# Kernel optimization log

Measured on AMD Instinct MI355X. Metric: run time of the kernel, lower is better.

## Reference

```python
import math
import jax, jax.numpy as jnp
import numpy as np

B, T, C = 2, 2048, 1024
HEADS = 16
HD = C // HEADS  # 64


def setup_inputs() -> dict:
    key = jax.random.key(0)
    ks = jax.random.split(key, 5)
    s = 0.02
    return {
        "x": jax.random.normal(ks[0], (B, T, C), jnp.float32),
        "Wq": jax.random.normal(ks[1], (C, C), jnp.float32) * s,
        "bq": jnp.zeros((C,), jnp.float32),
        "Wk": jax.random.normal(ks[2], (C, HD), jnp.float32) * s,
        "bk": jnp.zeros((HD,), jnp.float32),
        "Wv": jax.random.normal(ks[3], (C, HD), jnp.float32) * s,
        "bv": jnp.zeros((HD,), jnp.float32),
        "Wo": jax.random.normal(ks[4], (C, C), jnp.float32) * s,
        "bo": jnp.zeros((C,), jnp.float32),
    }


def _rope_tables(seq_len, dim):
    pos = jnp.arange(seq_len, dtype=jnp.float32)
    freqs = 1.0 / (10000.0 ** (jnp.arange(0, dim, 2, dtype=jnp.float32) / dim))
    ang = pos[:, None] * freqs[None, :]          # (T, dim//2)
    # broadcast over (B, T, H, dim//2)
    return jnp.sin(ang)[None, :, None, :], jnp.cos(ang)[None, :, None, :]


def _apply_rope(t, sin, cos, dim):
    t1, t2 = t[..., : dim // 2], t[..., dim // 2 :]
    # matches torch source: emb[..., :d/2]=sin, emb[..., d/2:]=cos
    return jnp.concatenate([t1 * cos + t2 * sin, t1 * sin - t2 * cos], axis=-1)


def reference(x, Wq, bq, Wk, bk, Wv, bv, Wo, bo):
    Bx, Tx, Cx = x.shape
    q = (x @ Wq + bq).reshape(Bx, Tx, HEADS, HD)   # (B,T,H,hd)
    k = (x @ Wk + bk)[:, :, None, :]               # (B,T,1,hd) single KV head (MQA)
    v = (x @ Wv + bv)[:, :, None, :]
    sin, cos = _rope_tables(Tx, HD)
    q = _apply_rope(q, sin, cos, HD)
    k = _apply_rope(k, sin, cos, HD)
    att = jnp.einsum('bthd,bThd->bhtT', q, k) / math.sqrt(HD)
    causal = jnp.triu(jnp.ones((Tx, Tx), bool), 1)
    att = jnp.where(causal, -jnp.inf, att)
    att = jax.nn.softmax(att, axis=-1)
    out = jnp.einsum('bhtT,bThd->bthd', att, v).reshape(Bx, Tx, Cx)
    return out @ Wo + bo
```

## Files before the change

kernel.cpp:

```cpp
#include <hip/hip_runtime.h>
#include <math.h>

#define BSZ   2
#define TSEQ  2048
#define CDIM  1024
#define NHEAD 16
#define HDIM  64
#define BT    (BSZ*TSEQ)
#define NQKV  1152

typedef __attribute__((ext_vector_type(8))) short short8;
typedef __attribute__((ext_vector_type(4))) float f32x4;
typedef unsigned short u16;
typedef unsigned int   u32;

__device__ __forceinline__ u16 f2b(float f) {
    union { float f; u32 u; } c; c.f = f;
    u32 u = c.u;
    u += 0x7fffu + ((u >> 16) & 1u);
    return (u16)(u >> 16);
}
__device__ __forceinline__ u32 pack2(float lo, float hi) {
    return (u32)f2b(lo) | ((u32)f2b(hi) << 16);
}

__device__ __forceinline__ void async_copy16(const void* g, void* l) {
    __builtin_amdgcn_global_load_lds(
        (__attribute__((address_space(1))) const void*)g,
        (__attribute__((address_space(3))) void*)l,
        16, 0, 0);
}

__global__ __launch_bounds__(256) void cast_bf16_kernel(
    const float* __restrict__ src, u16* __restrict__ dst, int n4)
{
    int i = blockIdx.x * 256 + threadIdx.x;
    if (i >= n4) return;
    float4 f = ((const float4*)src)[i];
    u16* d = dst + (size_t)i * 4;
    d[0] = f2b(f.x); d[1] = f2b(f.y); d[2] = f2b(f.z); d[3] = f2b(f.w);
}

__device__ __forceinline__ void transpose_tile(
    const float* __restrict__ W, u16* __restrict__ Wt,
    int K, int Nw, int nofs, int bx, int by, float (*T)[65])
{
    const int tid = threadIdx.x;
    const int k0 = by * 64, n0 = bx * 64;
    #pragma unroll
    for (int i = 0; i < 16; ++i) {
        int idx = i * 256 + tid, r = idx >> 6, c = idx & 63;
        T[r][c] = W[(size_t)(k0 + r) * Nw + n0 + c];
    }
    __syncthreads();
    #pragma unroll
    for (int i = 0; i < 16; ++i) {
        int idx = i * 256 + tid, rn = idx >> 6, ck = idx & 63;
        Wt[(size_t)(nofs + n0 + rn) * K + k0 + ck] = f2b(T[ck][rn]);
    }
}

__global__ __launch_bounds__(256) void prep_kernel(
    const float* __restrict__ Wq, const float* __restrict__ Wk,
    const float* __restrict__ Wv, const float* __restrict__ Wo,
    const float* __restrict__ bq, const float* __restrict__ bk,
    const float* __restrict__ bv,
    u16* __restrict__ Wqkvt, u16* __restrict__ Wot, float* __restrict__ bqkv)
{
    __shared__ float T[64][65];
    const int bid = blockIdx.x;
    if (bid < 256) {
        transpose_tile(Wq, Wqkvt, 1024, 1024, 0, bid & 15, bid >> 4, T);
    } else if (bid < 272) {
        transpose_tile(Wk, Wqkvt, 1024, 64, 1024, 0, bid - 256, T);
    } else if (bid < 288) {
        transpose_tile(Wv, Wqkvt, 1024, 64, 1088, 0, bid - 272, T);
    } else if (bid < 544) {
        int b2 = bid - 288;
        transpose_tile(Wo, Wot, 1024, 1024, 0, b2 & 15, b2 >> 4, T);
    } else {
        for (int i = threadIdx.x; i < NQKV; i += 256)
            bqkv[i] = (i < 1024) ? bq[i] : (i < 1088 ? bk[i - 1024] : bv[i - 1088]);
    }
}

__global__ __launch_bounds__(256) void gemm_qkv_kernel(
    const u16* __restrict__ A, const u16* __restrict__ Bt,
    const float* __restrict__ bias,
    u16* __restrict__ qb, u16* __restrict__ kb, u16* __restrict__ vT)
{
    __shared__ __align__(16) u16 AsC[64 * 32];
    __shared__ __align__(16) u16 BsC[128 * 32];
    const int tid  = threadIdx.x;
    const int wave = tid >> 6, lane = tid & 63;
    const int ln16 = lane & 15, quad = lane >> 4;
    const int wm = wave >> 1, wn = wave & 1;
    const int m0 = blockIdx.y * 64, n0 = blockIdx.x * 128;
    const int K = CDIM;

    const int c_row = ((tid >> 6) << 4) + (tid & 15);
    const int c_k   = ((tid >> 4) & 3) * 8;
    const u16* ag  = &A [(size_t)(m0 + c_row)       * K + c_k];
    const u16* bg0 = &Bt[(size_t)(n0 + c_row)       * K + c_k];
    const u16* bg1 = &Bt[(size_t)(n0 + 64 + c_row)  * K + c_k];
    u16* a_l  = &AsC[(size_t)wave * 64 * 8];
    u16* b_l0 = &BsC[(size_t)wave * 64 * 8];
    u16* b_l1 = &BsC[(size_t)(wave + 4) * 64 * 8];

    f32x4 acc[2][4];
    #pragma unroll
    for (int i = 0; i < 2; ++i)
        #pragma unroll
        for (int j = 0; j < 4; ++j) acc[i][j] = (f32x4){0.f, 0.f, 0.f, 0.f};

    for (int k0 = 0; k0 < K; k0 += 32) {
        async_copy16(ag,  a_l);
        async_copy16(bg0, b_l0);
        async_copy16(bg1, b_l1);
        ag += 32; bg0 += 32; bg1 += 32;
        __syncthreads();

        short8 af[2], bf[4];
        #pragma unroll
        for (int mt = 0; mt < 2; ++mt)
            af[mt] = *(const short8*)&AsC[(((wm * 2 + mt) * 64) + quad * 16 + ln16) * 8];
        #pragma unroll
        for (int nt = 0; nt < 4; ++nt)
            bf[nt] = *(const short8*)&BsC[(((wn * 4 + nt) * 64) + quad * 16 + ln16) * 8];
        #pragma unroll
        for (int mt = 0; mt < 2; ++mt)
            #pragma unroll
            for (int nt = 0; nt < 4; ++nt)
                acc[mt][nt] = __builtin_amdgcn_mfma_f32_16x16x32_bf16(
                    af[mt], bf[nt], acc[mt][nt], 0, 0, 0);
        __syncthreads();
    }

    #pragma unroll
    for (int mt = 0; mt < 2; ++mt)
        #pragma unroll
        for (int nt = 0; nt < 4; ++nt) {
            float bb = bias[n0 + wn * 64 + nt * 16 + ln16];
            #pragma unroll
            for (int r = 0; r < 4; ++r) acc[mt][nt][r] += bb;
        }

    const int col0 = n0 + wn * 64;
    if (col0 < 1024) {
        const int hh = col0 >> 6;
        #pragma unroll
        for (int nt = 0; nt < 2; ++nt) {
            int j = nt * 16 + ln16;
            float fr = exp2f(-0.41524101186092029f * (float)j);
            #pragma unroll
            for (int mt = 0; mt < 2; ++mt)
                #pragma unroll
                for (int r = 0; r < 4; ++r) {
                    int m = m0 + wm * 32 + mt * 16 + quad * 4 + r;
                    float sn, cs;
                    __sincosf((float)(m & (TSEQ - 1)) * fr, &sn, &cs);
                    float t1 = acc[mt][nt][r], t2 = acc[mt][nt + 2][r];
                    u16* o = qb + (size_t)m * CDIM + hh * 64 + j;
                    o[0]  = f2b(fmaf(t1, cs,  t2 * sn) * 0.125f);
                    o[32] = f2b(fmaf(t1, sn, -t2 * cs) * 0.125f);
                }
        }
    } else if (wn == 0) {
        #pragma unroll
        for (int nt = 0; nt < 2; ++nt) {
            int j = nt * 16 + ln16;
            float fr = exp2f(-0.41524101186092029f * (float)j);
            #pragma unroll
            for (int mt = 0; mt < 2; ++mt)
                #pragma unroll
                for (int r = 0; r < 4; ++r) {
                    int m = m0 + wm * 32 + mt * 16 + quad * 4 + r;
                    float sn, cs;
                    __sincosf((float)(m & (TSEQ - 1)) * fr, &sn, &cs);
                    float t1 = acc[mt][nt][r], t2 = acc[mt][nt + 2][r];
                    u16* o = kb + (size_t)m * HDIM + j;
                    o[0]  = f2b(fmaf(t1, cs,  t2 * sn));
                    o[32] = f2b(fmaf(t1, sn, -t2 * cs));
                }
        }
    } else {
        #pragma unroll
        for (int nt = 0; nt < 4; ++nt) {
            int d = nt * 16 + ln16;
            #pragma unroll
            for (int mt = 0; mt < 2; ++mt) {
                int mr = m0 + wm * 32 + mt * 16 + quad * 4;
                int b  = mr >> 11, tq = mr & (TSEQ - 1);
                uint2 val;
                val.x = pack2(acc[mt][nt][0], acc[mt][nt][1]);
                val.y = pack2(acc[mt][nt][2], acc[mt][nt][3]);
                *(uint2*)&vT[(size_t)(b * HDIM + d) * TSEQ + tq] = val;
            }
        }
    }
}

__global__ __launch_bounds__(256) void gemm_mfma_kernel(
    const u16* __restrict__ A, const u16* __restrict__ Bt,
    const float* __restrict__ bias, float* __restrict__ Y,
    int M, int N, int K)
{
    __shared__ __align__(16) u16 AsC[64 * 32];
    __shared__ __align__(16) u16 BsC[128 * 32];
    const int tid  = threadIdx.x;
    const int wave = tid >> 6, lane = tid & 63;
    const int ln16 = lane & 15, quad = lane >> 4;
    const int wm = wave >> 1, wn = wave & 1;
    const int m0 = blockIdx.y * 64, n0 = blockIdx.x * 128;

    const int c_row = ((tid >> 6) << 4) + (tid & 15);
    const int c_k   = ((tid >> 4) & 3) * 8;
    const u16* ag  = &A [(size_t)(m0 + c_row)       * K + c_k];
    const u16* bg0 = &Bt[(size_t)(n0 + c_row)       * K + c_k];
    const u16* bg1 = &Bt[(size_t)(n0 + 64 + c_row)  * K + c_k];
    u16* a_l  = &AsC[(size_t)wave * 64 * 8];
    u16* b_l0 = &BsC[(size_t)wave * 64 * 8];
    u16* b_l1 = &BsC[(size_t)(wave + 4) * 64 * 8];

    f32x4 acc[2][4];
    #pragma unroll
    for (int i = 0; i < 2; ++i)
        #pragma unroll
        for (int j = 0; j < 4; ++j) acc[i][j] = (f32x4){0.f, 0.f, 0.f, 0.f};

    for (int k0 = 0; k0 < K; k0 += 32) {
        async_copy16(ag,  a_l);
        async_copy16(bg0, b_l0);
        async_copy16(bg1, b_l1);
        ag += 32; bg0 += 32; bg1 += 32;
        __syncthreads();

        short8 af[2], bf[4];
        #pragma unroll
        for (int mt = 0; mt < 2; ++mt)
            af[mt] = *(const short8*)&AsC[(((wm * 2 + mt) * 64) + quad * 16 + ln16) * 8];
        #pragma unroll
        for (int nt = 0; nt < 4; ++nt)
            bf[nt] = *(const short8*)&BsC[(((wn * 4 + nt) * 64) + quad * 16 + ln16) * 8];
        #pragma unroll
        for (int mt = 0; mt < 2; ++mt)
            #pragma unroll
            for (int nt = 0; nt < 4; ++nt)
                acc[mt][nt] = __builtin_amdgcn_mfma_f32_16x16x32_bf16(
                    af[mt], bf[nt], acc[mt][nt], 0, 0, 0);
        __syncthreads();
    }

    #pragma unroll
    for (int mt = 0; mt < 2; ++mt)
        #pragma unroll
        for (int nt = 0; nt < 4; ++nt) {
            int n = n0 + wn * 64 + nt * 16 + ln16;
            float bb = bias[n];
            #pragma unroll
            for (int r = 0; r < 4; ++r) {
                int m = m0 + wm * 32 + mt * 16 + quad * 4 + r;
                Y[(size_t)m * N + n] = acc[mt][nt][r] + bb;
            }
        }
}

__global__ __launch_bounds__(256) void flash_mfma_kernel(
    const u16* __restrict__ qb, const u16* __restrict__ kb,
    const u16* __restrict__ vT, u16* __restrict__ o)
{
    const int id = blockIdx.x;
    const int p  = id & 15;
    const int h  = (id >> 4) & 15;
    const int b  = id >> 8;
    __shared__ __align__(16) u16 Qs[512 * 8];
    __shared__ __align__(16) u16 Ks[512 * 8];
    __shared__ __align__(16) u16 Vs[512 * 8];
    __shared__ __align__(16) u16 Ps[4 * 16 * 72];

    const int tid  = threadIdx.x;
    const int wave = tid >> 6, lane = tid & 63;
    const int ln16 = lane & 15, quad = lane >> 4;

    const int c0 = tid;
    int row_c[2], off_c[2];
    #pragma unroll
    for (int hf = 0; hf < 2; ++hf) {
        int c = c0 + hf * 256;
        row_c[hf] = ((c >> 7) << 4) | (c & 15);
        off_c[hf] = ((c >> 6) & 1) * 32 + ((c >> 4) & 3) * 8;
    }

    u16* Pw = &Ps[wave * 16 * 72];

    for (int s = 0; s < 2; ++s) {
        const int qt = s ? (31 - p) : p;

        #pragma unroll
        for (int hf = 0; hf < 2; ++hf)
            async_copy16(
                qb + (size_t)(b * TSEQ + qt * 64 + row_c[hf]) * CDIM + h * HDIM + off_c[hf],
                Qs + (c0 + hf * 256) * 8);

        float lsum[4];
        f32x4 oacc[4];
        #pragma unroll
        for (int r = 0; r < 4; ++r) lsum[r] = 0.f;
        #pragma unroll
        for (int t = 0; t < 4; ++t) oacc[t] = (f32x4){0.f, 0.f, 0.f, 0.f};

        for (int kt = 0; kt <= qt; ++kt) {
            const size_t kt0 = (size_t)(b * TSEQ + kt * 64);
            #pragma unroll
            for (int hf = 0; hf < 2; ++hf) {
                int cc = c0 + hf * 256;
                async_copy16(kb + (kt0 + row_c[hf]) * HDIM + off_c[hf], Ks + cc * 8);
                async_copy16(vT + (size_t)(b * HDIM + row_c[hf]) * TSEQ + kt * 64 + off_c[hf],
                             Vs + cc * 8);
            }
            __syncthreads();

            f32x4 sv[4];
            #pragma unroll
            for (int t = 0; t < 4; ++t) sv[t] = (f32x4){0.f, 0.f, 0.f, 0.f};
            #pragma unroll
            for (int kk2 = 0; kk2 < 2; ++kk2) {
                short8 af = *(const short8*)&Qs[(wave * 128 + kk2 * 64 + quad * 16 + ln16) * 8];
                #pragma unroll
                for (int t = 0; t < 4; ++t) {
                    short8 bf = *(const short8*)&Ks[(t * 128 + kk2 * 64 + quad * 16 + ln16) * 8];
                    sv[t] = __builtin_amdgcn_mfma_f32_16x16x32_bf16(af, bf, sv[t], 0, 0, 0);
                }
            }

            if (kt == qt) {
                #pragma unroll
                for (int t = 0; t < 4; ++t) {
                    int key = t * 16 + ln16;
                    #pragma unroll
                    for (int r = 0; r < 4; ++r) {
                        float e = (key > wave * 16 + quad * 4 + r)
                                    ? 0.f : __expf(sv[t][r]);
                        lsum[r] += e;
                        Pw[(quad * 4 + r) * 72 + t * 16 + ln16] = f2b(e);
                    }
                }
            } else {
                #pragma unroll
                for (int t = 0; t < 4; ++t)
                    #pragma unroll
                    for (int r = 0; r < 4; ++r) {
                        float e = __expf(sv[t][r]);
                        lsum[r] += e;
                        Pw[(quad * 4 + r) * 72 + t * 16 + ln16] = f2b(e);
                    }
            }

            #pragma unroll
            for (int kk2 = 0; kk2 < 2; ++kk2) {
                short8 pf = *(const short8*)&Pw[ln16 * 72 + kk2 * 32 + quad * 8];
                #pragma unroll
                for (int t = 0; t < 4; ++t) {
                    short8 vf = *(const short8*)&Vs[(t * 128 + kk2 * 64 + quad * 16 + ln16) * 8];
                    oacc[t] = __builtin_amdgcn_mfma_f32_16x16x32_bf16(pf, vf, oacc[t], 0, 0, 0);
                }
            }
            __syncthreads();
        }

        float inv[4];
        #pragma unroll
        for (int r = 0; r < 4; ++r) {
            float l = lsum[r];
            #pragma unroll
            for (int off = 1; off < 16; off <<= 1)
                l += __shfl_xor(l, off, 64);
            inv[r] = 1.0f / l;
        }
        #pragma unroll
        for (int t = 0; t < 4; ++t) {
            #pragma unroll
            for (int r = 0; r < 4; ++r) {
                int row = qt * 64 + wave * 16 + quad * 4 + r;
                int d   = t * 16 + ln16;
                o[(size_t)(b * TSEQ + row) * CDIM + h * HDIM + d] = f2b(oacc[t][r] * inv[r]);
            }
        }
    }
}

extern "C" void kernel_launch(void* const* d_in, const int* in_sizes, int n_in,
                              void* d_out, int out_size, void* d_ws, size_t ws_size,
                              hipStream_t stream)
{
    const float* x  = (const float*)d_in[0];
    const float* Wq = (const float*)d_in[1];
    const float* bq = (const float*)d_in[2];
    const float* Wk = (const float*)d_in[3];
    const float* bk = (const float*)d_in[4];
    const float* Wv = (const float*)d_in[5];
    const float* bv = (const float*)d_in[6];
    const float* Wo = (const float*)d_in[7];
    const float* bo = (const float*)d_in[8];
    float* out = (float*)d_out;

    const size_t MB = 1u << 20;
    char* w = (char*)d_ws;
    u16*   xb   = (u16*)(w);
    u16*   aob  = (u16*)(w);
    u16*   qb   = (u16*)(w + 8 * MB);
    u16*   kb   = (u16*)(w + 16 * MB);
    u16*   vT   = (u16*)(w + 16 * MB + 512 * 1024);
    u16*   Wqkvt= (u16*)(w + 17 * MB);
    u16*   Wot  = (u16*)(w + 20 * MB);
    float* bqkv = (float*)(w + 22 * MB);

    dim3 blk(256);

    cast_bf16_kernel<<<dim3(BT * CDIM / 4 / 256), blk, 0, stream>>>(x, xb, BT * CDIM / 4);
    prep_kernel<<<dim3(545), blk, 0, stream>>>(Wq, Wk, Wv, Wo, bq, bk, bv,
                                               Wqkvt, Wot, bqkv);
    gemm_qkv_kernel<<<dim3(NQKV / 128, BT / 64), blk, 0, stream>>>(
        xb, Wqkvt, bqkv, qb, kb, vT);
    flash_mfma_kernel<<<dim3(16 * NHEAD * BSZ), blk, 0, stream>>>(qb, kb, vT, aob);
    gemm_mfma_kernel<<<dim3(CDIM / 128, BT / 64), blk, 0, stream>>>(
        aob, Wot, bo, out, BT, CDIM, CDIM);
}
```

Before: 205.0 us.

## Shrink GEMM tiles to 64x64 with 2 waves and split flash work per query tile

Both GEMM kernels move from a 64x128 tile with 4 waves to a 64x64 tile with 2 waves, which doubles the block count so the 256 CUs are better filled. The flash attention kernel stops pairing a short and a long query tile in one block. It now launches one block per query tile, ordered longest-first to help load balance. In exchange, each GEMM block reuses less data, there are more launch blocks, and per-block causal work becomes uneven, which relies on the longest-first scheduling.

```diff
diff --git a/kernel.cpp b/kernel.cpp
--- a/kernel.cpp
+++ b/kernel.cpp
@@ -84,28 +84,31 @@
     }
 }
 
-__global__ __launch_bounds__(256) void gemm_qkv_kernel(
+__global__ __launch_bounds__(128) void gemm_qkv_kernel(
     const u16* __restrict__ A, const u16* __restrict__ Bt,
     const float* __restrict__ bias,
     u16* __restrict__ qb, u16* __restrict__ kb, u16* __restrict__ vT)
 {
     __shared__ __align__(16) u16 AsC[64 * 32];
-    __shared__ __align__(16) u16 BsC[128 * 32];
+    __shared__ __align__(16) u16 BsC[64 * 32];
     const int tid  = threadIdx.x;
     const int wave = tid >> 6, lane = tid & 63;
     const int ln16 = lane & 15, quad = lane >> 4;
-    const int wm = wave >> 1, wn = wave & 1;
-    const int m0 = blockIdx.y * 64, n0 = blockIdx.x * 128;
+    const int m0 = blockIdx.y * 64, n0 = blockIdx.x * 64;
     const int K = CDIM;
 
-    const int c_row = ((tid >> 6) << 4) + (tid & 15);
-    const int c_k   = ((tid >> 4) & 3) * 8;
-    const u16* ag  = &A [(size_t)(m0 + c_row)       * K + c_k];
-    const u16* bg0 = &Bt[(size_t)(n0 + c_row)       * K + c_k];
-    const u16* bg1 = &Bt[(size_t)(n0 + 64 + c_row)  * K + c_k];
-    u16* a_l  = &AsC[(size_t)wave * 64 * 8];
-    u16* b_l0 = &BsC[(size_t)wave * 64 * 8];
-    u16* b_l1 = &BsC[(size_t)(wave + 4) * 64 * 8];
+    const u16* ag[2]; u16* al[2];
+    const u16* bg[2]; u16* bl[2];
+    #pragma unroll
+    for (int n = 0; n < 2; ++n) {
+        int ca = tid + n * 128;
+        int row  = ((ca >> 6) << 4) | (ca & 15);
+        int koff = ((ca >> 4) & 3) * 8;
+        ag[n] = A  + (size_t)(m0 + row) * K + koff;
+        al[n] = AsC + ca * 8;
+        bg[n] = Bt + (size_t)(n0 + row) * K + koff;
+        bl[n] = BsC + ca * 8;
+    }
 
     f32x4 acc[2][4];
     #pragma unroll
@@ -114,19 +117,20 @@
         for (int j = 0; j < 4; ++j) acc[i][j] = (f32x4){0.f, 0.f, 0.f, 0.f};
 
     for (int k0 = 0; k0 < K; k0 += 32) {
-        async_copy16(ag,  a_l);
-        async_copy16(bg0, b_l0);
-        async_copy16(bg1, b_l1);
-        ag += 32; bg0 += 32; bg1 += 32;
+        #pragma unroll
+        for (int n = 0; n < 2; ++n) {
+            async_copy16(ag[n], al[n]); ag[n] += 32;
+            async_copy16(bg[n], bl[n]); bg[n] += 32;
+        }
         __syncthreads();
 
         short8 af[2], bf[4];
         #pragma unroll
         for (int mt = 0; mt < 2; ++mt)
-            af[mt] = *(const short8*)&AsC[(((wm * 2 + mt) * 64) + quad * 16 + ln16) * 8];
+            af[mt] = *(const short8*)&AsC[(((wave * 2 + mt) * 64) + lane) * 8];
         #pragma unroll
         for (int nt = 0; nt < 4; ++nt)
-            bf[nt] = *(const short8*)&BsC[(((wn * 4 + nt) * 64) + quad * 16 + ln16) * 8];
+            bf[nt] = *(const short8*)&BsC[((nt * 64) + lane) * 8];
         #pragma unroll
         for (int mt = 0; mt < 2; ++mt)
             #pragma unroll
@@ -137,17 +141,16 @@
     }
 
     #pragma unroll
-    for (int mt = 0; mt < 2; ++mt)
-        #pragma unroll
-        for (int nt = 0; nt < 4; ++nt) {
-            float bb = bias[n0 + wn * 64 + nt * 16 + ln16];
+    for (int nt = 0; nt < 4; ++nt) {
+        float bb = bias[n0 + nt * 16 + ln16];
+        #pragma unroll
+        for (int mt = 0; mt < 2; ++mt)
             #pragma unroll
             for (int r = 0; r < 4; ++r) acc[mt][nt][r] += bb;
-        }
-
-    const int col0 = n0 + wn * 64;
-    if (col0 < 1024) {
-        const int hh = col0 >> 6;
+    }
+
+    if (n0 < 1024) {
+        const int hh = n0 >> 6;
         #pragma unroll
         for (int nt = 0; nt < 2; ++nt) {
             int j = nt * 16 + ln16;
@@ -156,7 +159,7 @@
             for (int mt = 0; mt < 2; ++mt)
                 #pragma unroll
                 for (int r = 0; r < 4; ++r) {
-                    int m = m0 + wm * 32 + mt * 16 + quad * 4 + r;
+                    int m = m0 + wave * 32 + mt * 16 + quad * 4 + r;
                     float sn, cs;
                     __sincosf((float)(m & (TSEQ - 1)) * fr, &sn, &cs);
                     float t1 = acc[mt][nt][r], t2 = acc[mt][nt + 2][r];
@@ -165,7 +168,7 @@
                     o[32] = f2b(fmaf(t1, sn, -t2 * cs) * 0.125f);
                 }
         }
-    } else if (wn == 0) {
+    } else if (n0 == 1024) {
         #pragma unroll
         for (int nt = 0; nt < 2; ++nt) {
             int j = nt * 16 + ln16;
@@ -174,7 +177,7 @@
             for (int mt = 0; mt < 2; ++mt)
                 #pragma unroll
                 for (int r = 0; r < 4; ++r) {
-                    int m = m0 + wm * 32 + mt * 16 + quad * 4 + r;
+                    int m = m0 + wave * 32 + mt * 16 + quad * 4 + r;
                     float sn, cs;
                     __sincosf((float)(m & (TSEQ - 1)) * fr, &sn, &cs);
                     float t1 = acc[mt][nt][r], t2 = acc[mt][nt + 2][r];
@@ -189,7 +192,7 @@
             int d = nt * 16 + ln16;
             #pragma unroll
             for (int mt = 0; mt < 2; ++mt) {
-                int mr = m0 + wm * 32 + mt * 16 + quad * 4;
+                int mr = m0 + wave * 32 + mt * 16 + quad * 4;
                 int b  = mr >> 11, tq = mr & (TSEQ - 1);
                 uint2 val;
                 val.x = pack2(acc[mt][nt][0], acc[mt][nt][1]);
@@ -200,27 +203,30 @@
     }
 }
 
-__global__ __launch_bounds__(256) void gemm_mfma_kernel(
+__global__ __launch_bounds__(128) void gemm_mfma_kernel(
     const u16* __restrict__ A, const u16* __restrict__ Bt,
     const float* __restrict__ bias, float* __restrict__ Y,
     int M, int N, int K)
 {
     __shared__ __align__(16) u16 AsC[64 * 32];
-    __shared__ __align__(16) u16 BsC[128 * 32];
+    __shared__ __align__(16) u16 BsC[64 * 32];
     const int tid  = threadIdx.x;
     const int wave = tid >> 6, lane = tid & 63;
     const int ln16 = lane & 15, quad = lane >> 4;
-    const int wm = wave >> 1, wn = wave & 1;
-    const int m0 = blockIdx.y * 64, n0 = blockIdx.x * 128;
-
-    const int c_row = ((tid >> 6) << 4) + (tid & 15);
-    const int c_k   = ((tid >> 4) & 3) * 8;
-    const u16* ag  = &A [(size_t)(m0 + c_row)       * K + c_k];
-    const u16* bg0 = &Bt[(size_t)(n0 + c_row)       * K + c_k];
-    const u16* bg1 = &Bt[(size_t)(n0 + 64 + c_row)  * K + c_k];
-    u16* a_l  = &AsC[(size_t)wave * 64 * 8];
-    u16* b_l0 = &BsC[(size_t)wave * 64 * 8];
-    u16* b_l1 = &BsC[(size_t)(wave + 4) * 64 * 8];
+    const int m0 = blockIdx.y * 64, n0 = blockIdx.x * 64;
+
+    const u16* ag[2]; u16* al[2];
+    const u16* bg[2]; u16* bl[2];
+    #pragma unroll
+    for (int n = 0; n < 2; ++n) {
+        int ca = tid + n * 128;
+        int row  = ((ca >> 6) << 4) | (ca & 15);
+        int koff = ((ca >> 4) & 3) * 8;
+        ag[n] = A  + (size_t)(m0 + row) * K + koff;
+        al[n] = AsC + ca * 8;
+        bg[n] = Bt + (size_t)(n0 + row) * K + koff;
+        bl[n] = BsC + ca * 8;
+    }
 
     f32x4 acc[2][4];
     #pragma unroll
@@ -229,19 +235,20 @@
         for (int j = 0; j < 4; ++j) acc[i][j] = (f32x4){0.f, 0.f, 0.f, 0.f};
 
     for (int k0 = 0; k0 < K; k0 += 32) {
-        async_copy16(ag,  a_l);
-        async_copy16(bg0, b_l0);
-        async_copy16(bg1, b_l1);
-        ag += 32; bg0 += 32; bg1 += 32;
+        #pragma unroll
+        for (int n = 0; n < 2; ++n) {
+            async_copy16(ag[n], al[n]); ag[n] += 32;
+            async_copy16(bg[n], bl[n]); bg[n] += 32;
+        }
         __syncthreads();
 
         short8 af[2], bf[4];
         #pragma unroll
         for (int mt = 0; mt < 2; ++mt)
-            af[mt] = *(const short8*)&AsC[(((wm * 2 + mt) * 64) + quad * 16 + ln16) * 8];
+            af[mt] = *(const short8*)&AsC[(((wave * 2 + mt) * 64) + lane) * 8];
         #pragma unroll
         for (int nt = 0; nt < 4; ++nt)
-            bf[nt] = *(const short8*)&BsC[(((wn * 4 + nt) * 64) + quad * 16 + ln16) * 8];
+            bf[nt] = *(const short8*)&BsC[((nt * 64) + lane) * 8];
         #pragma unroll
         for (int mt = 0; mt < 2; ++mt)
             #pragma unroll
@@ -252,27 +259,28 @@
     }
 
     #pragma unroll
-    for (int mt = 0; mt < 2; ++mt)
-        #pragma unroll
-        for (int nt = 0; nt < 4; ++nt) {
-            int n = n0 + wn * 64 + nt * 16 + ln16;
-            float bb = bias[n];
+    for (int nt = 0; nt < 4; ++nt) {
+        int n = n0 + nt * 16 + ln16;
+        float bb = bias[n];
+        #pragma unroll
+        for (int mt = 0; mt < 2; ++mt)
             #pragma unroll
             for (int r = 0; r < 4; ++r) {
-                int m = m0 + wm * 32 + mt * 16 + quad * 4 + r;
+                int m = m0 + wave * 32 + mt * 16 + quad * 4 + r;
                 Y[(size_t)m * N + n] = acc[mt][nt][r] + bb;
             }
-        }
+    }
 }
 
 __global__ __launch_bounds__(256) void flash_mfma_kernel(
     const u16* __restrict__ qb, const u16* __restrict__ kb,
     const u16* __restrict__ vT, u16* __restrict__ o)
 {
-    const int id = blockIdx.x;
-    const int p  = id & 15;
-    const int h  = (id >> 4) & 15;
-    const int b  = id >> 8;
+    const int id  = blockIdx.x;
+    const int qt  = 31 - (id >> 5);
+    const int hb  = id & 31;
+    const int h   = hb >> 1;
+    const int b   = hb & 1;
     __shared__ __align__(16) u16 Qs[512 * 8];
     __shared__ __align__(16) u16 Ks[512 * 8];
     __shared__ __align__(16) u16 Vs[512 * 8];
@@ -293,98 +301,94 @@
 
     u16* Pw = &Ps[wave * 16 * 72];
 
-    for (int s = 0; s < 2; ++s) {
-        const int qt = s ? (31 - p) : p;
-
-        #pragma unroll
-        for (int hf = 0; hf < 2; ++hf)
-            async_copy16(
-                qb + (size_t)(b * TSEQ + qt * 64 + row_c[hf]) * CDIM + h * HDIM + off_c[hf],
-                Qs + (c0 + hf * 256) * 8);
-
-        float lsum[4];
-        f32x4 oacc[4];
-        #pragma unroll
-        for (int r = 0; r < 4; ++r) lsum[r] = 0.f;
-        #pragma unroll
-        for (int t = 0; t < 4; ++t) oacc[t] = (f32x4){0.f, 0.f, 0.f, 0.f};
-
-        for (int kt = 0; kt <= qt; ++kt) {
-            const size_t kt0 = (size_t)(b * TSEQ + kt * 64);
-            #pragma unroll
-            for (int hf = 0; hf < 2; ++hf) {
-                int cc = c0 + hf * 256;
-                async_copy16(kb + (kt0 + row_c[hf]) * HDIM + off_c[hf], Ks + cc * 8);
-                async_copy16(vT + (size_t)(b * HDIM + row_c[hf]) * TSEQ + kt * 64 + off_c[hf],
-                             Vs + cc * 8);
+    #pragma unroll
+    for (int hf = 0; hf < 2; ++hf)
+        async_copy16(
+            qb + (size_t)(b * TSEQ + qt * 64 + row_c[hf]) * CDIM + h * HDIM + off_c[hf],
+            Qs + (c0 + hf * 256) * 8);
+
+    float lsum[4];
+    f32x4 oacc[4];
+    #pragma unroll
+    for (int r = 0; r < 4; ++r) lsum[r] = 0.f;
+    #pragma unroll
+    for (int t = 0; t < 4; ++t) oacc[t] = (f32x4){0.f, 0.f, 0.f, 0.f};
+
+    for (int kt = 0; kt <= qt; ++kt) {
+        const size_t kt0 = (size_t)(b * TSEQ + kt * 64);
+        #pragma unroll
+        for (int hf = 0; hf < 2; ++hf) {
+            int cc = c0 + hf * 256;
+            async_copy16(kb + (kt0 + row_c[hf]) * HDIM + off_c[hf], Ks + cc * 8);
+            async_copy16(vT + (size_t)(b * HDIM + row_c[hf]) * TSEQ + kt * 64 + off_c[hf],
+                         Vs + cc * 8);
+        }
+        __syncthreads();
+
+        f32x4 sv[4];
+        #pragma unroll
+        for (int t = 0; t < 4; ++t) sv[t] = (f32x4){0.f, 0.f, 0.f, 0.f};
+        #pragma unroll
+        for (int kk2 = 0; kk2 < 2; ++kk2) {
+            short8 af = *(const short8*)&Qs[(wave * 128 + kk2 * 64 + quad * 16 + ln16) * 8];
+            #pragma unroll
+            for (int t = 0; t < 4; ++t) {
+                short8 bf = *(const short8*)&Ks[(t * 128 + kk2 * 64 + quad * 16 + ln16) * 8];
+                sv[t] = __builtin_amdgcn_mfma_f32_16x16x32_bf16(af, bf, sv[t], 0, 0, 0);
             }
-            __syncthreads();
-
-            f32x4 sv[4];
-            #pragma unroll
-            for (int t = 0; t < 4; ++t) sv[t] = (f32x4){0.f, 0.f, 0.f, 0.f};
-            #pragma unroll
-            for (int kk2 = 0; kk2 < 2; ++kk2) {
-                short8 af = *(const short8*)&Qs[(wave * 128 + kk2 * 64 + quad * 16 + ln16) * 8];
+        }
+
+        if (kt == qt) {
+            #pragma unroll
+            for (int t = 0; t < 4; ++t) {
+                int key = t * 16 + ln16;
                 #pragma unroll
-                for (int t = 0; t < 4; ++t) {
-                    short8 bf = *(const short8*)&Ks[(t * 128 + kk2 * 64 + quad * 16 + ln16) * 8];
-                    sv[t] = __builtin_amdgcn_mfma_f32_16x16x32_bf16(af, bf, sv[t], 0, 0, 0);
+                for (int r = 0; r < 4; ++r) {
+                    float e = (key > wave * 16 + quad * 4 + r)
+                                ? 0.f : __expf(sv[t][r]);
+                    lsum[r] += e;
+                    Pw[(quad * 4 + r) * 72 + t * 16 + ln16] = f2b(e);
                 }
             }
-
-            if (kt == qt) {
+        } else {
+            #pragma unroll
+            for (int t = 0; t < 4; ++t)
                 #pragma unroll
-                for (int t = 0; t < 4; ++t) {
-                    int key = t * 16 + ln16;
-                    #pragma unroll
-                    for (int r = 0; r < 4; ++r) {
-                        float e = (key > wave * 16 + quad * 4 + r)
-                                    ? 0.f : __expf(sv[t][r]);
-                        lsum[r] += e;
-                        Pw[(quad * 4 + r) * 72 + t * 16 + ln16] = f2b(e);
-                    }
+                for (int r = 0; r < 4; ++r) {
+                    float e = __expf(sv[t][r]);
+                    lsum[r] += e;
+                    Pw[(quad * 4 + r) * 72 + t * 16 + ln16] = f2b(e);
                 }
-            } else {
-                #pragma unroll
-                for (int t = 0; t < 4; ++t)
-                    #pragma unroll
-                    for (int r = 0; r < 4; ++r) {
-                        float e = __expf(sv[t][r]);
-                        lsum[r] += e;
-                        Pw[(quad * 4 + r) * 72 + t * 16 + ln16] = f2b(e);
-                    }
+        }
+
+        #pragma unroll
+        for (int kk2 = 0; kk2 < 2; ++kk2) {
+            short8 pf = *(const short8*)&Pw[ln16 * 72 + kk2 * 32 + quad * 8];
+            #pragma unroll
+            for (int t = 0; t < 4; ++t) {
+                short8 vf = *(const short8*)&Vs[(t * 128 + kk2 * 64 + quad * 16 + ln16) * 8];
+                oacc[t] = __builtin_amdgcn_mfma_f32_16x16x32_bf16(pf, vf, oacc[t], 0, 0, 0);
             }
-
-            #pragma unroll
-            for (int kk2 = 0; kk2 < 2; ++kk2) {
-                short8 pf = *(const short8*)&Pw[ln16 * 72 + kk2 * 32 + quad * 8];
-                #pragma unroll
-                for (int t = 0; t < 4; ++t) {
-                    short8 vf = *(const short8*)&Vs[(t * 128 + kk2 * 64 + quad * 16 + ln16) * 8];
-                    oacc[t] = __builtin_amdgcn_mfma_f32_16x16x32_bf16(pf, vf, oacc[t], 0, 0, 0);
-                }
-            }
-            __syncthreads();
-        }
-
-        float inv[4];
+        }
+        __syncthreads();
+    }
+
+    float inv[4];
+    #pragma unroll
+    for (int r = 0; r < 4; ++r) {
+        float l = lsum[r];
+        #pragma unroll
+        for (int off = 1; off < 16; off <<= 1)
+            l += __shfl_xor(l, off, 64);
+        inv[r] = 1.0f / l;
+    }
+    #pragma unroll
+    for (int t = 0; t < 4; ++t) {
         #pragma unroll
         for (int r = 0; r < 4; ++r) {
-            float l = lsum[r];
-            #pragma unroll
-            for (int off = 1; off < 16; off <<= 1)
-                l += __shfl_xor(l, off, 64);
-            inv[r] = 1.0f / l;
-        }
-        #pragma unroll
-        for (int t = 0; t < 4; ++t) {
-            #pragma unroll
-            for (int r = 0; r < 4; ++r) {
-                int row = qt * 64 + wave * 16 + quad * 4 + r;
-                int d   = t * 16 + ln16;
-                o[(size_t)(b * TSEQ + row) * CDIM + h * HDIM + d] = f2b(oacc[t][r] * inv[r]);
-            }
+            int row = qt * 64 + wave * 16 + quad * 4 + r;
+            int d   = t * 16 + ln16;
+            o[(size_t)(b * TSEQ + row) * CDIM + h * HDIM + d] = f2b(oacc[t][r] * inv[r]);
         }
     }
 }
@@ -415,14 +419,14 @@
     u16*   Wot  = (u16*)(w + 20 * MB);
     float* bqkv = (float*)(w + 22 * MB);
 
-    dim3 blk(256);
-
-    cast_bf16_kernel<<<dim3(BT * CDIM / 4 / 256), blk, 0, stream>>>(x, xb, BT * CDIM / 4);
-    prep_kernel<<<dim3(545), blk, 0, stream>>>(Wq, Wk, Wv, Wo, bq, bk, bv,
-                                               Wqkvt, Wot, bqkv);
-    gemm_qkv_kernel<<<dim3(NQKV / 128, BT / 64), blk, 0, stream>>>(
+    cast_bf16_kernel<<<dim3(BT * CDIM / 4 / 256), dim3(256), 0, stream>>>(
+        x, xb, BT * CDIM / 4);
+    prep_kernel<<<dim3(545), dim3(256), 0, stream>>>(Wq, Wk, Wv, Wo, bq, bk, bv,
+                                                     Wqkvt, Wot, bqkv);
+    gemm_qkv_kernel<<<dim3(NQKV / 64, BT / 64), dim3(128), 0, stream>>>(
         xb, Wqkvt, bqkv, qb, kb, vT);
-    flash_mfma_kernel<<<dim3(16 * NHEAD * BSZ), blk, 0, stream>>>(qb, kb, vT, aob);
-    gemm_mfma_kernel<<<dim3(CDIM / 128, BT / 64), blk, 0, stream>>>(
+    flash_mfma_kernel<<<dim3(32 * NHEAD * BSZ), dim3(256), 0, stream>>>(
+        qb, kb, vT, aob);
+    gemm_mfma_kernel<<<dim3(CDIM / 64, BT / 64), dim3(128), 0, stream>>>(
         aob, Wot, bo, out, BT, CDIM, CDIM);
 }
```

Result: slower. 212.4 us (+3.6%).

## Double-buffer K/V tiles in flash kernel and schedule one query tile per block

Applied to the files above, without the earlier changes.

Splits the flash attention work so each block handles a single query tile, launched longest-first, instead of a balanced pair of tiles per block. It adds a second K/V shared-memory buffer so the next tile's async copy overlaps the current tile's compute. It also folds log2(e) into the Q scale so exp2f replaces __expf. The trade-offs are more shared memory per block, twice as many blocks, and reliance on launch order to balance causal work.

```diff
diff --git a/kernel.cpp b/kernel.cpp
--- a/kernel.cpp
+++ b/kernel.cpp
@@ -161,8 +161,8 @@
                     __sincosf((float)(m & (TSEQ - 1)) * fr, &sn, &cs);
                     float t1 = acc[mt][nt][r], t2 = acc[mt][nt + 2][r];
                     u16* o = qb + (size_t)m * CDIM + hh * 64 + j;
-                    o[0]  = f2b(fmaf(t1, cs,  t2 * sn) * 0.125f);
-                    o[32] = f2b(fmaf(t1, sn, -t2 * cs) * 0.125f);
+                    o[0]  = f2b(fmaf(t1, cs,  t2 * sn) * 0.18033688011112043f);
+                    o[32] = f2b(fmaf(t1, sn, -t2 * cs) * 0.18033688011112043f);
                 }
         }
     } else if (wn == 0) {
@@ -265,17 +265,87 @@
         }
 }
 
+__device__ __forceinline__ void flash_stage_kv(
+    const u16* __restrict__ kb, const u16* __restrict__ vT,
+    int b, int kt, u16* __restrict__ Ksb, u16* __restrict__ Vsb,
+    const int* row_c, const int* off_c, int c0)
+{
+    const size_t kt0 = (size_t)(b * TSEQ + kt * 64);
+    #pragma unroll
+    for (int hf = 0; hf < 2; ++hf) {
+        int cc = c0 + hf * 256;
+        async_copy16(kb + (kt0 + row_c[hf]) * HDIM + off_c[hf], Ksb + cc * 8);
+        async_copy16(vT + (size_t)(b * HDIM + row_c[hf]) * TSEQ + kt * 64 + off_c[hf],
+                     Vsb + cc * 8);
+    }
+}
+
+__device__ __forceinline__ void flash_tile(
+    const u16* __restrict__ Ksb, const u16* __restrict__ Vsb,
+    const u16* __restrict__ Qs, u16* __restrict__ Pw,
+    int wave, int ln16, int quad, bool diag,
+    float* lsum, f32x4* oacc)
+{
+    f32x4 sv[4];
+    #pragma unroll
+    for (int t = 0; t < 4; ++t) sv[t] = (f32x4){0.f, 0.f, 0.f, 0.f};
+    #pragma unroll
+    for (int kk2 = 0; kk2 < 2; ++kk2) {
+        short8 af = *(const short8*)&Qs[(wave * 128 + kk2 * 64 + quad * 16 + ln16) * 8];
+        #pragma unroll
+        for (int t = 0; t < 4; ++t) {
+            short8 bf = *(const short8*)&Ksb[(t * 128 + kk2 * 64 + quad * 16 + ln16) * 8];
+            sv[t] = __builtin_amdgcn_mfma_f32_16x16x32_bf16(af, bf, sv[t], 0, 0, 0);
+        }
+    }
+
+    if (diag) {
+        #pragma unroll
+        for (int t = 0; t < 4; ++t) {
+            int key = t * 16 + ln16;
+            #pragma unroll
+            for (int r = 0; r < 4; ++r) {
+                float e = (key > wave * 16 + quad * 4 + r) ? 0.f : exp2f(sv[t][r]);
+                lsum[r] += e;
+                Pw[(quad * 4 + r) * 72 + t * 16 + ln16] = f2b(e);
+            }
+        }
+    } else {
+        #pragma unroll
+        for (int t = 0; t < 4; ++t)
+            #pragma unroll
+            for (int r = 0; r < 4; ++r) {
+                float e = exp2f(sv[t][r]);
+                lsum[r] += e;
+                Pw[(quad * 4 + r) * 72 + t * 16 + ln16] = f2b(e);
+            }
+    }
+
+    #pragma unroll
+    for (int kk2 = 0; kk2 < 2; ++kk2) {
+        short8 pf = *(const short8*)&Pw[ln16 * 72 + kk2 * 32 + quad * 8];
+        #pragma unroll
+        for (int t = 0; t < 4; ++t) {
+            short8 vf = *(const short8*)&Vsb[(t * 128 + kk2 * 64 + quad * 16 + ln16) * 8];
+            oacc[t] = __builtin_amdgcn_mfma_f32_16x16x32_bf16(pf, vf, oacc[t], 0, 0, 0);
+        }
+    }
+}
+
 __global__ __launch_bounds__(256) void flash_mfma_kernel(
     const u16* __restrict__ qb, const u16* __restrict__ kb,
     const u16* __restrict__ vT, u16* __restrict__ o)
 {
-    const int id = blockIdx.x;
-    const int p  = id & 15;
-    const int h  = (id >> 4) & 15;
-    const int b  = id >> 8;
-    __shared__ __align__(16) u16 Qs[512 * 8];
-    __shared__ __align__(16) u16 Ks[512 * 8];
-    __shared__ __align__(16) u16 Vs[512 * 8];
+    const int id  = blockIdx.x;
+    const int qt  = 31 - (id >> 5);
+    const int hb  = id & 31;
+    const int h   = hb >> 1;
+    const int b   = hb & 1;
+    __shared__ __align__(16) u16 Qs [512 * 8];
+    __shared__ __align__(16) u16 Ks0[512 * 8];
+    __shared__ __align__(16) u16 Ks1[512 * 8];
+    __shared__ __align__(16) u16 Vs0[512 * 8];
+    __shared__ __align__(16) u16 Vs1[512 * 8];
     __shared__ __align__(16) u16 Ps[4 * 16 * 72];
 
     const int tid  = threadIdx.x;
@@ -293,98 +363,48 @@
 
     u16* Pw = &Ps[wave * 16 * 72];
 
-    for (int s = 0; s < 2; ++s) {
-        const int qt = s ? (31 - p) : p;
-
-        #pragma unroll
-        for (int hf = 0; hf < 2; ++hf)
-            async_copy16(
-                qb + (size_t)(b * TSEQ + qt * 64 + row_c[hf]) * CDIM + h * HDIM + off_c[hf],
-                Qs + (c0 + hf * 256) * 8);
-
-        float lsum[4];
-        f32x4 oacc[4];
-        #pragma unroll
-        for (int r = 0; r < 4; ++r) lsum[r] = 0.f;
-        #pragma unroll
-        for (int t = 0; t < 4; ++t) oacc[t] = (f32x4){0.f, 0.f, 0.f, 0.f};
-
-        for (int kt = 0; kt <= qt; ++kt) {
-            const size_t kt0 = (size_t)(b * TSEQ + kt * 64);
-            #pragma unroll
-            for (int hf = 0; hf < 2; ++hf) {
-                int cc = c0 + hf * 256;
-                async_copy16(kb + (kt0 + row_c[hf]) * HDIM + off_c[hf], Ks + cc * 8);
-                async_copy16(vT + (size_t)(b * HDIM + row_c[hf]) * TSEQ + kt * 64 + off_c[hf],
-                             Vs + cc * 8);
-            }
-            __syncthreads();
-
-            f32x4 sv[4];
-            #pragma unroll
-            for (int t = 0; t < 4; ++t) sv[t] = (f32x4){0.f, 0.f, 0.f, 0.f};
-            #pragma unroll
-            for (int kk2 = 0; kk2 < 2; ++kk2) {
-                short8 af = *(const short8*)&Qs[(wave * 128 + kk2 * 64 + quad * 16 + ln16) * 8];
-                #pragma unroll
-                for (int t = 0; t < 4; ++t) {
-                    short8 bf = *(const short8*)&Ks[(t * 128 + kk2 * 64 + quad * 16 + ln16) * 8];
-                    sv[t] = __builtin_amdgcn_mfma_f32_16x16x32_bf16(af, bf, sv[t], 0, 0, 0);
-                }
-            }
-
-            if (kt == qt) {
-                #pragma unroll
-                for (int t = 0; t < 4; ++t) {
-                    int key = t * 16 + ln16;
-                    #pragma unroll
-                    for (int r = 0; r < 4; ++r) {
-                        float e = (key > wave * 16 + quad * 4 + r)
-                                    ? 0.f : __expf(sv[t][r]);
-                        lsum[r] += e;
-                        Pw[(quad * 4 + r) * 72 + t * 16 + ln16] = f2b(e);
-                    }
-                }
-            } else {
-                #pragma unroll
-                for (int t = 0; t < 4; ++t)
-                    #pragma unroll
-                    for (int r = 0; r < 4; ++r) {
-                        float e = __expf(sv[t][r]);
-                        lsum[r] += e;
-                        Pw[(quad * 4 + r) * 72 + t * 16 + ln16] = f2b(e);
-                    }
-            }
-
-            #pragma unroll
-            for (int kk2 = 0; kk2 < 2; ++kk2) {
-                short8 pf = *(const short8*)&Pw[ln16 * 72 + kk2 * 32 + quad * 8];
-                #pragma unroll
-                for (int t = 0; t < 4; ++t) {
-                    short8 vf = *(const short8*)&Vs[(t * 128 + kk2 * 64 + quad * 16 + ln16) * 8];
-                    oacc[t] = __builtin_amdgcn_mfma_f32_16x16x32_bf16(pf, vf, oacc[t], 0, 0, 0);
-                }
-            }
-            __syncthreads();
-        }
-
-        float inv[4];
+    #pragma unroll
+    for (int hf = 0; hf < 2; ++hf)
+        async_copy16(
+            qb + (size_t)(b * TSEQ + qt * 64 + row_c[hf]) * CDIM + h * HDIM + off_c[hf],
+            Qs + (c0 + hf * 256) * 8);
+    flash_stage_kv(kb, vT, b, 0, Ks0, Vs0, row_c, off_c, c0);
+
+    float lsum[4];
+    f32x4 oacc[4];
+    #pragma unroll
+    for (int r = 0; r < 4; ++r) lsum[r] = 0.f;
+    #pragma unroll
+    for (int t = 0; t < 4; ++t) oacc[t] = (f32x4){0.f, 0.f, 0.f, 0.f};
+
+    int kt = 0;
+    while (true) {
+        __syncthreads();
+        if (kt < qt) flash_stage_kv(kb, vT, b, kt + 1, Ks1, Vs1, row_c, off_c, c0);
+        flash_tile(Ks0, Vs0, Qs, Pw, wave, ln16, quad, kt == qt, lsum, oacc);
+        if (++kt > qt) break;
+        __syncthreads();
+        if (kt < qt) flash_stage_kv(kb, vT, b, kt + 1, Ks0, Vs0, row_c, off_c, c0);
+        flash_tile(Ks1, Vs1, Qs, Pw, wave, ln16, quad, kt == qt, lsum, oacc);
+        if (++kt > qt) break;
+    }
+
+    float inv[4];
+    #pragma unroll
+    for (int r = 0; r < 4; ++r) {
+        float l = lsum[r];
+        #pragma unroll
+        for (int off = 1; off < 16; off <<= 1)
+            l += __shfl_xor(l, off, 64);
+        inv[r] = 1.0f / l;
+    }
+    #pragma unroll
+    for (int t = 0; t < 4; ++t) {
         #pragma unroll
         for (int r = 0; r < 4; ++r) {
-            float l = lsum[r];
-            #pragma unroll
-            for (int off = 1; off < 16; off <<= 1)
-                l += __shfl_xor(l, off, 64);
-            inv[r] = 1.0f / l;
-        }
-        #pragma unroll
-        for (int t = 0; t < 4; ++t) {
-            #pragma unroll
-            for (int r = 0; r < 4; ++r) {
-                int row = qt * 64 + wave * 16 + quad * 4 + r;
-                int d   = t * 16 + ln16;
-                o[(size_t)(b * TSEQ + row) * CDIM + h * HDIM + d] = f2b(oacc[t][r] * inv[r]);
-            }
+            int row = qt * 64 + wave * 16 + quad * 4 + r;
+            int d   = t * 16 + ln16;
+            o[(size_t)(b * TSEQ + row) * CDIM + h * HDIM + d] = f2b(oacc[t][r] * inv[r]);
         }
     }
 }
@@ -415,14 +435,14 @@
     u16*   Wot  = (u16*)(w + 20 * MB);
     float* bqkv = (float*)(w + 22 * MB);
 
-    dim3 blk(256);
-
-    cast_bf16_kernel<<<dim3(BT * CDIM / 4 / 256), blk, 0, stream>>>(x, xb, BT * CDIM / 4);
-    prep_kernel<<<dim3(545), blk, 0, stream>>>(Wq, Wk, Wv, Wo, bq, bk, bv,
-                                               Wqkvt, Wot, bqkv);
-    gemm_qkv_kernel<<<dim3(NQKV / 128, BT / 64), blk, 0, stream>>>(
+    cast_bf16_kernel<<<dim3(BT * CDIM / 4 / 256), dim3(256), 0, stream>>>(
+        x, xb, BT * CDIM / 4);
+    prep_kernel<<<dim3(545), dim3(256), 0, stream>>>(Wq, Wk, Wv, Wo, bq, bk, bv,
+                                                     Wqkvt, Wot, bqkv);
+    gemm_qkv_kernel<<<dim3(NQKV / 128, BT / 64), dim3(256), 0, stream>>>(
         xb, Wqkvt, bqkv, qb, kb, vT);
-    flash_mfma_kernel<<<dim3(16 * NHEAD * BSZ), blk, 0, stream>>>(qb, kb, vT, aob);
-    gemm_mfma_kernel<<<dim3(CDIM / 128, BT / 64), blk, 0, stream>>>(
+    flash_mfma_kernel<<<dim3(32 * NHEAD * BSZ), dim3(256), 0, stream>>>(
+        qb, kb, vT, aob);
+    gemm_mfma_kernel<<<dim3(CDIM / 128, BT / 64), dim3(256), 0, stream>>>(
         aob, Wot, bo, out, BT, CDIM, CDIM);
 }
```

Result: faster. 192.7 us (-6.0%).
